# Optimization experiments

Hardware: AMD Instinct MI355X
Metric: run time of the kernel (lower is better)

The kernel has to match this reference:

```python
import jax, jax.numpy as jnp
import numpy as np

NUM_BUSES = 20000
NUM_LINES = 320000
OTHER = 1000
BATCH = 128


def setup_inputs() -> dict:
    key = jax.random.key(0)
    k1, k2, k3, k4, k5 = jax.random.split(key, 5)
    x = jax.random.normal(k1, (BATCH, 2 * NUM_BUSES + OTHER), dtype=jnp.float32)
    from_indices = jax.random.randint(k2, (NUM_LINES,), 0, NUM_BUSES, dtype=jnp.int32)
    to_indices = jax.random.randint(k3, (NUM_LINES,), 0, NUM_BUSES, dtype=jnp.int32)
    # reactances bounded away from 0 (realistic p.u. line reactances)
    reactances = 0.01 + 0.2 * jax.random.uniform(k4, (NUM_LINES,), dtype=jnp.float32)
    limits = 0.5 + 1.5 * jax.random.uniform(k5, (NUM_LINES,), dtype=jnp.float32)
    return {
        "x": x,
        "from_indices": from_indices,
        "to_indices": to_indices,
        "reactances": reactances,
        "limits": limits,
        "num_buses": NUM_BUSES,
    }


def reference(x, from_indices, to_indices, reactances, limits, num_buses):
    nb = num_buses
    voltages = x[:, :nb]                     # [B, nb]
    angles = x[:, nb:2 * nb]                 # [B, nb]
    other_params = x[:, 2 * nb:]             # [B, other]

    from_a = angles[:, from_indices]         # [B, L] gather
    to_a = angles[:, to_indices]
    angle_diffs = from_a - to_a
    flows = angle_diffs / reactances[None, :]
    over = jnp.abs(flows / limits[None, :]) > 1.0

    # Torch runs this branch only if any line is over limit; when none are,
    # adjustments are identically zero, so applying unconditionally is exact.
    required = jnp.sign(angle_diffs) * (reactances * limits)[None, :]
    adjustments = jnp.where(over, required, angle_diffs) - angle_diffs  # [B, L]
    half = adjustments * 0.5
    # angles = angles + from_adjustments - to_adjustments
    #        = angles + scatter_add(from, adj/2) + scatter_add(to, adj/2)
    # (torch accumulates -adj/2 into to_adjustments, then subtracts it)
    delta = jnp.zeros_like(angles).at[:, from_indices].add(half).at[:, to_indices].add(half)
    angles2 = angles + delta

    diffs2 = angles2[:, from_indices] - angles2[:, to_indices]
    flows2 = diffs2 / reactances[None, :]

    out = jnp.concatenate([voltages, angles2, other_params], axis=1)
    return out, flows2
```

## Files before the change

kernel.cpp:

```cpp
#include <hip/hip_runtime.h>

#define NB     20000
#define NL     320000
#define NOTH   1000
#define BATCH  128
#define ROW    (2*NB + NOTH)
#define CAP    80
#define BCHUNK 8
#define CB     (NB/BCHUNK)
#define NSLICE 2
#define LPS    (NL/NSLICE)

__device__ __forceinline__ float fast_rcp(float a)
{
    float r;
    asm volatile("v_rcp_f32 %0, %1" : "=v"(r) : "v"(a));
    return r;
}

__global__ __launch_bounds__(256) void zero_k(int* __restrict__ cnt)
{
    const int i = blockIdx.x * 256 + threadIdx.x;
    if (i < NB / 4) ((int4*)cnt)[i] = make_int4(0, 0, 0, 0);
}

__global__ __launch_bounds__(256) void build_k(
    const int* __restrict__ fidx, const int* __restrict__ tidx,
    const float* __restrict__ xr, const float* __restrict__ lim,
    int* __restrict__ cnt, unsigned* __restrict__ bins)
{
    const int q = blockIdx.x * 256 + threadIdx.x;
    if (q >= NL / 4) return;
    const int4   f = ((const int4*)fidx)[q];
    const int4   t = ((const int4*)tidx)[q];
    const float4 r = ((const float4*)xr)[q];
    const float4 L = ((const float4*)lim)[q];

    #define EMIT(FI, TI, RC, LC)                                             \
    {                                                                        \
        union { float f; unsigned u; } c; c.f = (RC) * (LC);                 \
        const unsigned rl16 = (c.u + 0x8000u) >> 16;                         \
        const int p0 = atomicAdd(&cnt[FI], 1);                               \
        if (p0 < CAP) bins[(size_t)p0 * NB + (FI)] =                         \
            ((unsigned)(TI) << 17) | rl16;                                   \
        const int p1 = atomicAdd(&cnt[TI], 1);                               \
        if (p1 < CAP) bins[(size_t)p1 * NB + (TI)] =                         \
            ((unsigned)(FI) << 17) | (1u << 16) | rl16;                      \
    }
    EMIT(f.x, t.x, r.x, L.x)
    EMIT(f.y, t.y, r.y, L.y)
    EMIT(f.z, t.z, r.z, L.z)
    EMIT(f.w, t.w, r.w, L.w)
    #undef EMIT
}

__device__ __forceinline__ float contrib(unsigned w, float ab, const float* a)
{
    const int   other = (int)(w >> 17);
    const float rl    = __uint_as_float((w & 0xFFFFu) << 16);
    const float ad    = ab - a[other];
    float h = 0.0f;
    if (fabsf(ad) > rl) {
        h = 0.5f * (copysignf(rl, ad) - ad);
        if (w & (1u << 16)) h = -h;
    }
    return h;
}

__global__ __launch_bounds__(1024) void delta_copy_k(
    const float* __restrict__ x, const int* __restrict__ cnt,
    const unsigned* __restrict__ bins, float* __restrict__ out)
{
    extern __shared__ float a[];
    const int b  = blockIdx.x % BATCH;
    const int cb = blockIdx.x / BATCH;

    const float* __restrict__ xrow = x   + (size_t)b * ROW;
    float*       __restrict__ orow = out + (size_t)b * ROW;

    for (int i = threadIdx.x; i < NB / 4; i += 1024)
        ((float4*)a)[i] = ((const float4*)(xrow + NB))[i];
    __syncthreads();

    for (int i = threadIdx.x; i < CB / 4; i += 1024)
        ((float4*)(orow + cb * CB))[i] = ((const float4*)(xrow + cb * CB))[i];
    if (cb == 0)
        for (int i = threadIdx.x; i < NOTH / 4; i += 1024)
            ((float4*)(orow + 2 * NB))[i] = ((const float4*)(xrow + 2 * NB))[i];

    const int base = cb * CB;
    for (int bus = base + (int)threadIdx.x; bus < base + CB; bus += 1024) {
        const int   n  = min(cnt[bus], CAP);
        const float ab = a[bus];
        float ds = 0.0f;
        int k = 0;
        for (; k + 4 <= n; k += 4) {
            const unsigned w0 = bins[(size_t)(k + 0) * NB + bus];
            const unsigned w1 = bins[(size_t)(k + 1) * NB + bus];
            const unsigned w2 = bins[(size_t)(k + 2) * NB + bus];
            const unsigned w3 = bins[(size_t)(k + 3) * NB + bus];
            ds += contrib(w0, ab, a) + contrib(w1, ab, a)
                + contrib(w2, ab, a) + contrib(w3, ab, a);
        }
        for (; k < n; ++k)
            ds += contrib(bins[(size_t)k * NB + bus], ab, a);
        orow[NB + bus] = ab + ds;
    }
}

__global__ __launch_bounds__(1024) void flows_lds_k(
    const float* __restrict__ out, const int* __restrict__ fidx,
    const int* __restrict__ tidx, const float* __restrict__ xr,
    float* __restrict__ f2)
{
    extern __shared__ float a2[];
    const int b = blockIdx.x % BATCH;
    const int s = blockIdx.x / BATCH;

    const float* __restrict__ src = out + (size_t)b * ROW + NB;
    for (int i = threadIdx.x; i < NB / 4; i += 1024)
        ((float4*)a2)[i] = ((const float4*)src)[i];
    __syncthreads();

    float* __restrict__ frow = f2 + (size_t)b * NL;
    const int q0 = s * (LPS / 4);
    const int q1 = q0 + (LPS / 4);
    for (int q = q0 + (int)threadIdx.x; q < q1; q += 1024) {
        const int4   f = ((const int4*)fidx)[q];
        const int4   t = ((const int4*)tidx)[q];
        const float4 r = ((const float4*)xr)[q];
        float4 o;
        o.x = (a2[f.x] - a2[t.x]) * fast_rcp(r.x);
        o.y = (a2[f.y] - a2[t.y]) * fast_rcp(r.y);
        o.z = (a2[f.z] - a2[t.z]) * fast_rcp(r.z);
        o.w = (a2[f.w] - a2[t.w]) * fast_rcp(r.w);
        ((float4*)frow)[q] = o;
    }
}

extern "C" void kernel_launch(void* const* d_in, const int* in_sizes, int n_in,
                              void* d_out, int out_size, void* d_ws, size_t ws_size,
                              hipStream_t stream)
{
    const float* x   = (const float*)d_in[0];
    const int*   fi  = (const int*)  d_in[1];
    const int*   ti  = (const int*)  d_in[2];
    const float* xr  = (const float*)d_in[3];
    const float* lim = (const float*)d_in[4];

    float* out    = (float*)d_out;
    float* flows2 = out + (size_t)BATCH * ROW;

    int*      cnt  = (int*)d_ws;
    unsigned* bins = (unsigned*)((char*)d_ws + NB * 4);

    zero_k<<<dim3((NB / 4 + 255) / 256), dim3(256), 0, stream>>>(cnt);

    build_k<<<dim3((NL / 4 + 255) / 256), dim3(256), 0, stream>>>(
        fi, ti, xr, lim, cnt, bins);

    delta_copy_k<<<dim3(BCHUNK * BATCH), dim3(1024), NB * 4, stream>>>(
        x, cnt, bins, out);

    flows_lds_k<<<dim3(NSLICE * BATCH), dim3(1024), NB * 4, stream>>>(
        out, fi, ti, xr, flows2);
}
```

Measured before the change: 128.2 us.

## Process four batch rows per block with bf16 LDS angles and padded counters

Each block now handles four batch rows at once, keeping their angle vectors in shared memory as bf16, so one read of the bin entries and edge indices serves four rows. Bus counters are padded to separate cache lines to reduce atomic contention in the build step, and flow outputs use nontemporal stores with more slices. Storing angles as bf16 loses precision in both the over-limit test and the recomputed flows, which can break accuracy tolerances.

```diff
diff --git a/kernel.cpp b/kernel.cpp
--- a/kernel.cpp
+++ b/kernel.cpp
@@ -6,10 +6,15 @@
 #define BATCH  128
 #define ROW    (2*NB + NOTH)
 #define CAP    80
+#define PAD    16
+#define RPB    4
+#define NGRP   (BATCH/RPB)
 #define BCHUNK 8
 #define CB     (NB/BCHUNK)
-#define NSLICE 2
+#define NSLICE 8
 #define LPS    (NL/NSLICE)
+
+typedef float vf4 __attribute__((ext_vector_type(4)));
 
 __device__ __forceinline__ float fast_rcp(float a)
 {
@@ -17,11 +22,19 @@
     asm volatile("v_rcp_f32 %0, %1" : "=v"(r) : "v"(a));
     return r;
 }
+__device__ __forceinline__ float bf2f(ushort u)
+{
+    union { uint i; float f; } c; c.i = ((uint)u) << 16; return c.f;
+}
+__device__ __forceinline__ ushort f2bf(float f)
+{
+    union { uint i; float f; } c; c.f = f; return (ushort)((c.i + 0x8000u) >> 16);
+}
 
 __global__ __launch_bounds__(256) void zero_k(int* __restrict__ cnt)
 {
     const int i = blockIdx.x * 256 + threadIdx.x;
-    if (i < NB / 4) ((int4*)cnt)[i] = make_int4(0, 0, 0, 0);
+    if (i < NB * PAD / 4) ((int4*)cnt)[i] = make_int4(0, 0, 0, 0);
 }
 
 __global__ __launch_bounds__(256) void build_k(
@@ -40,10 +53,10 @@
     {                                                                        \
         union { float f; unsigned u; } c; c.f = (RC) * (LC);                 \
         const unsigned rl16 = (c.u + 0x8000u) >> 16;                         \
-        const int p0 = atomicAdd(&cnt[FI], 1);                               \
+        const int p0 = atomicAdd(&cnt[(FI) * PAD], 1);                       \
         if (p0 < CAP) bins[(size_t)p0 * NB + (FI)] =                         \
             ((unsigned)(TI) << 17) | rl16;                                   \
-        const int p1 = atomicAdd(&cnt[TI], 1);                               \
+        const int p1 = atomicAdd(&cnt[(TI) * PAD], 1);                       \
         if (p1 < CAP) bins[(size_t)p1 * NB + (TI)] =                         \
             ((unsigned)(FI) << 17) | (1u << 16) | rl16;                      \
     }
@@ -54,57 +67,60 @@
     #undef EMIT
 }
 
-__device__ __forceinline__ float contrib(unsigned w, float ab, const float* a)
-{
-    const int   other = (int)(w >> 17);
-    const float rl    = __uint_as_float((w & 0xFFFFu) << 16);
-    const float ad    = ab - a[other];
-    float h = 0.0f;
-    if (fabsf(ad) > rl) {
-        h = 0.5f * (copysignf(rl, ad) - ad);
-        if (w & (1u << 16)) h = -h;
-    }
-    return h;
-}
-
 __global__ __launch_bounds__(1024) void delta_copy_k(
     const float* __restrict__ x, const int* __restrict__ cnt,
     const unsigned* __restrict__ bins, float* __restrict__ out)
 {
-    extern __shared__ float a[];
-    const int b  = blockIdx.x % BATCH;
-    const int cb = blockIdx.x / BATCH;
+    extern __shared__ ushort a4[];
+    const int g  = blockIdx.x % NGRP;
+    const int cb = blockIdx.x / NGRP;
+    const int row0 = g * RPB;
 
-    const float* __restrict__ xrow = x   + (size_t)b * ROW;
-    float*       __restrict__ orow = out + (size_t)b * ROW;
-
-    for (int i = threadIdx.x; i < NB / 4; i += 1024)
-        ((float4*)a)[i] = ((const float4*)(xrow + NB))[i];
+    for (int i = threadIdx.x; i < RPB * (NB / 4); i += 1024) {
+        const int r = i / (NB / 4), j = i % (NB / 4);
+        const float4 v = ((const float4*)(x + (size_t)(row0 + r) * ROW + NB))[j];
+        ushort4 u;
+        u.x = f2bf(v.x); u.y = f2bf(v.y); u.z = f2bf(v.z); u.w = f2bf(v.w);
+        ((ushort4*)a4)[i] = u;
+    }
     __syncthreads();
 
-    for (int i = threadIdx.x; i < CB / 4; i += 1024)
-        ((float4*)(orow + cb * CB))[i] = ((const float4*)(xrow + cb * CB))[i];
-    if (cb == 0)
-        for (int i = threadIdx.x; i < NOTH / 4; i += 1024)
-            ((float4*)(orow + 2 * NB))[i] = ((const float4*)(xrow + 2 * NB))[i];
+    for (int r = 0; r < RPB; ++r) {
+        const float* __restrict__ xrow = x   + (size_t)(row0 + r) * ROW;
+        float*       __restrict__ orow = out + (size_t)(row0 + r) * ROW;
+        for (int i = threadIdx.x; i < CB / 4; i += 1024)
+            ((float4*)(orow + cb * CB))[i] = ((const float4*)(xrow + cb * CB))[i];
+        if (cb == 0)
+            for (int i = threadIdx.x; i < NOTH / 4; i += 1024)
+                ((float4*)(orow + 2 * NB))[i] = ((const float4*)(xrow + 2 * NB))[i];
+    }
 
     const int base = cb * CB;
     for (int bus = base + (int)threadIdx.x; bus < base + CB; bus += 1024) {
-        const int   n  = min(cnt[bus], CAP);
-        const float ab = a[bus];
-        float ds = 0.0f;
-        int k = 0;
-        for (; k + 4 <= n; k += 4) {
-            const unsigned w0 = bins[(size_t)(k + 0) * NB + bus];
-            const unsigned w1 = bins[(size_t)(k + 1) * NB + bus];
-            const unsigned w2 = bins[(size_t)(k + 2) * NB + bus];
-            const unsigned w3 = bins[(size_t)(k + 3) * NB + bus];
-            ds += contrib(w0, ab, a) + contrib(w1, ab, a)
-                + contrib(w2, ab, a) + contrib(w3, ab, a);
+        const int n = min(cnt[bus * PAD], CAP);
+        float ab[RPB], ds[RPB];
+        #pragma unroll
+        for (int r = 0; r < RPB; ++r) {
+            ab[r] = bf2f(a4[r * NB + bus]);
+            ds[r] = 0.0f;
         }
-        for (; k < n; ++k)
-            ds += contrib(bins[(size_t)k * NB + bus], ab, a);
-        orow[NB + bus] = ab + ds;
+        for (int k = 0; k < n; ++k) {
+            const unsigned w  = bins[(size_t)k * NB + bus];
+            const int   other = (int)(w >> 17);
+            const float rl    = __uint_as_float((w & 0xFFFFu) << 16);
+            const float sgn   = (w & (1u << 16)) ? -0.5f : 0.5f;
+            #pragma unroll
+            for (int r = 0; r < RPB; ++r) {
+                const float ad = ab[r] - bf2f(a4[r * NB + other]);
+                if (fabsf(ad) > rl)
+                    ds[r] += sgn * (copysignf(rl, ad) - ad);
+            }
+        }
+        #pragma unroll
+        for (int r = 0; r < RPB; ++r) {
+            const size_t o = (size_t)(row0 + r) * ROW + NB + bus;
+            out[o] = x[o] + ds[r];
+        }
     }
 }
 
@@ -113,28 +129,39 @@
     const int* __restrict__ tidx, const float* __restrict__ xr,
     float* __restrict__ f2)
 {
-    extern __shared__ float a2[];
-    const int b = blockIdx.x % BATCH;
-    const int s = blockIdx.x / BATCH;
+    extern __shared__ ushort a4[];
+    const int g = blockIdx.x % NGRP;
+    const int s = blockIdx.x / NGRP;
+    const int row0 = g * RPB;
 
-    const float* __restrict__ src = out + (size_t)b * ROW + NB;
-    for (int i = threadIdx.x; i < NB / 4; i += 1024)
-        ((float4*)a2)[i] = ((const float4*)src)[i];
+    for (int i = threadIdx.x; i < RPB * (NB / 4); i += 1024) {
+        const int r = i / (NB / 4), j = i % (NB / 4);
+        const float4 v = ((const float4*)(out + (size_t)(row0 + r) * ROW + NB))[j];
+        ushort4 u;
+        u.x = f2bf(v.x); u.y = f2bf(v.y); u.z = f2bf(v.z); u.w = f2bf(v.w);
+        ((ushort4*)a4)[i] = u;
+    }
     __syncthreads();
 
-    float* __restrict__ frow = f2 + (size_t)b * NL;
     const int q0 = s * (LPS / 4);
     const int q1 = q0 + (LPS / 4);
     for (int q = q0 + (int)threadIdx.x; q < q1; q += 1024) {
         const int4   f = ((const int4*)fidx)[q];
         const int4   t = ((const int4*)tidx)[q];
         const float4 r = ((const float4*)xr)[q];
-        float4 o;
-        o.x = (a2[f.x] - a2[t.x]) * fast_rcp(r.x);
-        o.y = (a2[f.y] - a2[t.y]) * fast_rcp(r.y);
-        o.z = (a2[f.z] - a2[t.z]) * fast_rcp(r.z);
-        o.w = (a2[f.w] - a2[t.w]) * fast_rcp(r.w);
-        ((float4*)frow)[q] = o;
+        const float4 ir = make_float4(fast_rcp(r.x), fast_rcp(r.y),
+                                      fast_rcp(r.z), fast_rcp(r.w));
+        #pragma unroll
+        for (int rr = 0; rr < RPB; ++rr) {
+            const ushort* __restrict__ a = a4 + rr * NB;
+            vf4 o;
+            o.x = (bf2f(a[f.x]) - bf2f(a[t.x])) * ir.x;
+            o.y = (bf2f(a[f.y]) - bf2f(a[t.y])) * ir.y;
+            o.z = (bf2f(a[f.z]) - bf2f(a[t.z])) * ir.z;
+            o.w = (bf2f(a[f.w]) - bf2f(a[t.w])) * ir.w;
+            __builtin_nontemporal_store(
+                o, &((vf4*)(f2 + (size_t)(row0 + rr) * NL))[q]);
+        }
     }
 }
 
@@ -152,16 +179,16 @@
     float* flows2 = out + (size_t)BATCH * ROW;
 
     int*      cnt  = (int*)d_ws;
-    unsigned* bins = (unsigned*)((char*)d_ws + NB * 4);
+    unsigned* bins = (unsigned*)((char*)d_ws + (size_t)NB * PAD * 4);
 
-    zero_k<<<dim3((NB / 4 + 255) / 256), dim3(256), 0, stream>>>(cnt);
+    zero_k<<<dim3((NB * PAD / 4 + 255) / 256), dim3(256), 0, stream>>>(cnt);
 
     build_k<<<dim3((NL / 4 + 255) / 256), dim3(256), 0, stream>>>(
         fi, ti, xr, lim, cnt, bins);
 
-    delta_copy_k<<<dim3(BCHUNK * BATCH), dim3(1024), NB * 4, stream>>>(
-        x, cnt, bins, out);
+    delta_copy_k<<<dim3(BCHUNK * NGRP), dim3(1024),
+                   RPB * NB * sizeof(ushort), stream>>>(x, cnt, bins, out);
 
-    flows_lds_k<<<dim3(NSLICE * BATCH), dim3(1024), NB * 4, stream>>>(
-        out, fi, ti, xr, flows2);
+    flows_lds_k<<<dim3(NSLICE * NGRP), dim3(1024),
+                  RPB * NB * sizeof(ushort), stream>>>(out, fi, ti, xr, flows2);
 }
```

After: 139.4 us. +8.7%, slower.

## Build per-bus adjacency bins via block-local histogram, scan, and LDS placement

Applied to the files above, without the earlier changes.

Replaces the global-atomic bin construction with a three-pass counting sort. Each of 256 blocks builds a shared-memory histogram of its line segment, a column scan turns these into per-block prefix offsets, and a placement pass writes bins using LDS atomics plus those offsets. This removes contention on global atomics and makes slot order deterministic, at the cost of two extra launches and a 10 MB ushort histogram in the workspace. The contribution helper is also inlined as a macro that only accumulates when a line is over its limit. The old path is kept as a fallback when the workspace is too small.

```diff
diff --git a/kernel.cpp b/kernel.cpp
--- a/kernel.cpp
+++ b/kernel.cpp
@@ -6,6 +6,8 @@
 #define BATCH  128
 #define ROW    (2*NB + NOTH)
 #define CAP    80
+#define NBLK   256
+#define LSEG   (NL/NBLK)
 #define BCHUNK 8
 #define CB     (NB/BCHUNK)
 #define NSLICE 2
@@ -16,6 +18,72 @@
     float r;
     asm volatile("v_rcp_f32 %0, %1" : "=v"(r) : "v"(a));
     return r;
+}
+
+__global__ __launch_bounds__(512) void histo_k(
+    const int* __restrict__ fidx, const int* __restrict__ tidx,
+    ushort* __restrict__ H)
+{
+    extern __shared__ uint h[];
+    for (int i = threadIdx.x; i < NB; i += 512) h[i] = 0u;
+    __syncthreads();
+
+    const int l0 = blockIdx.x * LSEG;
+    for (int l = l0 + (int)threadIdx.x; l < l0 + LSEG; l += 512) {
+        atomicAdd(&h[fidx[l]], 1u);
+        atomicAdd(&h[tidx[l]], 1u);
+    }
+    __syncthreads();
+
+    ushort* __restrict__ Hrow = H + (size_t)blockIdx.x * NB;
+    for (int i = threadIdx.x; i < NB / 2; i += 512) {
+        ushort2 u; u.x = (ushort)h[2 * i]; u.y = (ushort)h[2 * i + 1];
+        ((ushort2*)Hrow)[i] = u;
+    }
+}
+
+__global__ __launch_bounds__(512) void scan_k(
+    ushort* __restrict__ H, int* __restrict__ cnt)
+{
+    const int u = blockIdx.x * 512 + threadIdx.x;
+    if (u >= NB) return;
+    uint run = 0;
+    for (int b = 0; b < NBLK; ++b) {
+        const uint v = H[(size_t)b * NB + u];
+        H[(size_t)b * NB + u] = (ushort)run;
+        run += v;
+    }
+    cnt[u] = (int)run;
+}
+
+__global__ __launch_bounds__(512) void place_k(
+    const int* __restrict__ fidx, const int* __restrict__ tidx,
+    const float* __restrict__ xr, const float* __restrict__ lim,
+    const ushort* __restrict__ H, unsigned* __restrict__ bins)
+{
+    extern __shared__ char sm[];
+    uint*   __restrict__ h    = (uint*)sm;
+    ushort* __restrict__ pref = (ushort*)(sm + NB * 4);
+
+    const ushort* __restrict__ Hrow = H + (size_t)blockIdx.x * NB;
+    for (int i = threadIdx.x; i < NB; i += 512) h[i] = 0u;
+    for (int i = threadIdx.x; i < NB / 2; i += 512)
+        ((ushort2*)pref)[i] = ((const ushort2*)Hrow)[i];
+    __syncthreads();
+
+    const int l0 = blockIdx.x * LSEG;
+    for (int l = l0 + (int)threadIdx.x; l < l0 + LSEG; l += 512) {
+        const int fi = fidx[l];
+        const int ti = tidx[l];
+        union { float f; unsigned u; } c; c.f = xr[l] * lim[l];
+        const unsigned rl16 = (c.u + 0x8000u) >> 16;
+
+        const uint s0 = (uint)pref[fi] + atomicAdd(&h[fi], 1u);
+        if (s0 < CAP) bins[(size_t)s0 * NB + fi] = ((unsigned)ti << 17) | rl16;
+        const uint s1 = (uint)pref[ti] + atomicAdd(&h[ti], 1u);
+        if (s1 < CAP) bins[(size_t)s1 * NB + ti] =
+            ((unsigned)fi << 17) | (1u << 16) | rl16;
+    }
 }
 
 __global__ __launch_bounds__(256) void zero_k(int* __restrict__ cnt)
@@ -35,7 +103,6 @@
     const int4   t = ((const int4*)tidx)[q];
     const float4 r = ((const float4*)xr)[q];
     const float4 L = ((const float4*)lim)[q];
-
     #define EMIT(FI, TI, RC, LC)                                             \
     {                                                                        \
         union { float f; unsigned u; } c; c.f = (RC) * (LC);                 \
@@ -54,19 +121,6 @@
     #undef EMIT
 }
 
-__device__ __forceinline__ float contrib(unsigned w, float ab, const float* a)
-{
-    const int   other = (int)(w >> 17);
-    const float rl    = __uint_as_float((w & 0xFFFFu) << 16);
-    const float ad    = ab - a[other];
-    float h = 0.0f;
-    if (fabsf(ad) > rl) {
-        h = 0.5f * (copysignf(rl, ad) - ad);
-        if (w & (1u << 16)) h = -h;
-    }
-    return h;
-}
-
 __global__ __launch_bounds__(1024) void delta_copy_k(
     const float* __restrict__ x, const int* __restrict__ cnt,
     const unsigned* __restrict__ bins, float* __restrict__ out)
@@ -94,16 +148,27 @@
         const float ab = a[bus];
         float ds = 0.0f;
         int k = 0;
+        #define CONTRIB(W)                                                   \
+        {                                                                    \
+            const unsigned w  = (W);                                         \
+            const int   other = (int)(w >> 17);                              \
+            const float rl    = __uint_as_float((w & 0xFFFFu) << 16);        \
+            const float ad    = ab - a[other];                               \
+            if (fabsf(ad) > rl) {                                            \
+                float hh = 0.5f * (copysignf(rl, ad) - ad);                  \
+                if (w & (1u << 16)) hh = -hh;                                \
+                ds += hh;                                                    \
+            }                                                                \
+        }
         for (; k + 4 <= n; k += 4) {
             const unsigned w0 = bins[(size_t)(k + 0) * NB + bus];
             const unsigned w1 = bins[(size_t)(k + 1) * NB + bus];
             const unsigned w2 = bins[(size_t)(k + 2) * NB + bus];
             const unsigned w3 = bins[(size_t)(k + 3) * NB + bus];
-            ds += contrib(w0, ab, a) + contrib(w1, ab, a)
-                + contrib(w2, ab, a) + contrib(w3, ab, a);
+            CONTRIB(w0) CONTRIB(w1) CONTRIB(w2) CONTRIB(w3)
         }
-        for (; k < n; ++k)
-            ds += contrib(bins[(size_t)k * NB + bus], ab, a);
+        for (; k < n; ++k) CONTRIB(bins[(size_t)k * NB + bus])
+        #undef CONTRIB
         orow[NB + bus] = ab + ds;
     }
 }
@@ -151,17 +216,33 @@
     float* out    = (float*)d_out;
     float* flows2 = out + (size_t)BATCH * ROW;
 
-    int*      cnt  = (int*)d_ws;
-    unsigned* bins = (unsigned*)((char*)d_ws + NB * 4);
-
-    zero_k<<<dim3((NB / 4 + 255) / 256), dim3(256), 0, stream>>>(cnt);
-
-    build_k<<<dim3((NL / 4 + 255) / 256), dim3(256), 0, stream>>>(
-        fi, ti, xr, lim, cnt, bins);
-
-    delta_copy_k<<<dim3(BCHUNK * BATCH), dim3(1024), NB * 4, stream>>>(
+    const size_t hBytes = (size_t)NBLK * NB * sizeof(ushort);
+    const size_t needed = hBytes + (size_t)NB * 4 + (size_t)CAP * NB * 4;
+
+    int* cnt;
+    unsigned* bins;
+
+    if (ws_size >= needed) {
+        ushort* H = (ushort*)d_ws;
+        cnt  = (int*)((char*)d_ws + hBytes);
+        bins = (unsigned*)((char*)d_ws + hBytes + (size_t)NB * 4);
+
+        histo_k<<<dim3(NBLK), dim3(512), NB * sizeof(uint), stream>>>(fi, ti, H);
+        scan_k<<<dim3((NB + 511) / 512), dim3(512), 0, stream>>>(H, cnt);
+        place_k<<<dim3(NBLK), dim3(512),
+                  NB * sizeof(uint) + NB * sizeof(ushort), stream>>>(
+            fi, ti, xr, lim, H, bins);
+    } else {
+        cnt  = (int*)d_ws;
+        bins = (unsigned*)((char*)d_ws + (size_t)NB * 4);
+        zero_k<<<dim3((NB / 4 + 255) / 256), dim3(256), 0, stream>>>(cnt);
+        build_k<<<dim3((NL / 4 + 255) / 256), dim3(256), 0, stream>>>(
+            fi, ti, xr, lim, cnt, bins);
+    }
+
+    delta_copy_k<<<dim3(BCHUNK * BATCH), dim3(1024), NB * sizeof(float), stream>>>(
         x, cnt, bins, out);
 
-    flows_lds_k<<<dim3(NSLICE * BATCH), dim3(1024), NB * 4, stream>>>(
+    flows_lds_k<<<dim3(NSLICE * BATCH), dim3(1024), NB * sizeof(float), stream>>>(
         out, fi, ti, xr, flows2);
 }
```

New measurement: 116.2 us. -9.4%, faster.
